# Kernel tuning notes

Measured on AMD Instinct MI355X. Metric: run time of the kernel, lower is better.

Reference implementation:

```python
import jax, jax.numpy as jnp
import numpy as np

N = 50000      # nodes
E = 800000     # edges
B = 512        # graphs in batch
DRNL = 64      # drnl_dim (feature_dim = 0)
H = 256        # hidden


def setup_inputs() -> dict:
    key = jax.random.key(0)
    ks = jax.random.split(key, 12)
    x = jax.random.normal(ks[0], (N, DRNL), jnp.float32)
    edge_index = jax.random.randint(ks[1], (2, E), 0, N)
    batch_vec = jnp.sort(jax.random.randint(ks[2], (N,), 0, B))
    u_idx = jax.random.randint(ks[3], (B,), 0, N)
    v_idx = jax.random.randint(ks[4], (B,), 0, N)

    def glorot(k, shp):
        scale = jnp.sqrt(2.0 / (shp[0] + shp[1]))
        return (jax.random.normal(k, shp, jnp.float32) * scale).astype(jnp.float32)

    W0 = glorot(ks[5], (DRNL, H)); b0 = jnp.zeros((H,), jnp.float32)
    W1 = glorot(ks[6], (H, H));    b1 = jnp.zeros((H,), jnp.float32)
    W2 = glorot(ks[7], (H, H));    b2 = jnp.zeros((H,), jnp.float32)
    Wm1 = glorot(ks[8], (3 * H, H)); bm1 = jnp.zeros((H,), jnp.float32)
    Wm2 = glorot(ks[9], (H, 1));     bm2 = jnp.zeros((1,), jnp.float32)
    return dict(x=x, edge_index=edge_index, batch_vec=batch_vec,
                u_idx=u_idx, v_idx=v_idx,
                W0=W0, b0=b0, W1=W1, b1=b1, W2=W2, b2=b2,
                Wm1=Wm1, bm1=bm1, Wm2=Wm2, bm2=bm2)


def _gcn_encode(x, src, dst, Ws, bs):
    # Standard GCN: h' = D^-1/2 (A + I) D^-1/2 h W + b, ReLU between layers.
    n = x.shape[0]
    loop = jnp.arange(n)
    src2 = jnp.concatenate([src, loop])  # add self-loops
    dst2 = jnp.concatenate([dst, loop])
    deg = jax.ops.segment_sum(jnp.ones_like(dst2, x.dtype), dst2, num_segments=n)
    dis = jax.lax.rsqrt(jnp.maximum(deg, 1.0))          # D^-1/2
    norm = dis[src2] * dis[dst2]                         # per-edge norm [E+N]

    h = x
    for i, (W, b) in enumerate(zip(Ws, bs)):
        msg = h[src2] * norm[:, None]                    # gather + scale
        agg = jax.ops.segment_sum(msg, dst2, num_segments=n)
        h = agg @ W + b
        if i < len(Ws) - 1:
            h = jax.nn.relu(h)
    return h


def reference(x, edge_index, batch_vec, u_idx, v_idx,
              W0, b0, W1, b1, W2, b2, Wm1, bm1, Wm2, bm2):
    src, dst = edge_index[0], edge_index[1]
    h = _gcn_encode(x, src, dst, (W0, W1, W2), (b0, b1, b2))   # [N, H]

    # global_mean_pool over batch_vec -> [B, H]
    cnt = jax.ops.segment_sum(jnp.ones((h.shape[0],), h.dtype), batch_vec,
                              num_segments=B)
    g = jax.ops.segment_sum(h, batch_vec, num_segments=B) / \
        jnp.maximum(cnt, 1.0)[:, None]

    # concat [g, h[u], h[v]] -> MLP -> [B] logits
    z = jnp.concatenate([g, h[u_idx], h[v_idx]], axis=1)       # [B, 3H]
    z = jax.nn.relu(z @ Wm1 + bm1)
    return (z @ Wm2 + bm2).squeeze(-1)
```

## Files before the change

### kernel.cpp

```cpp
#include <hip/hip_runtime.h>
#include <hip/hip_bf16.h>
#include <stdint.h>

#ifndef DRNL
#define DRNL 64
#define HDIM 256
#endif

#define CHUNK 4096
#define BCAP 3072

typedef __attribute__((ext_vector_type(4))) float f32x4;
typedef __attribute__((ext_vector_type(8))) _Float16 f16x8;

__device__ __forceinline__ int imin(int a, int b) { return a < b ? a : b; }

__global__ __launch_bounds__(256) void k_misc(
    const int* __restrict__ batch,
    const float* __restrict__ x,
    const float* __restrict__ W0, const float* __restrict__ W1,
    const float* __restrict__ W2,
    int* __restrict__ gstart,
    _Float16* __restrict__ x16,
    _Float16* __restrict__ W0t, _Float16* __restrict__ W1t,
    _Float16* __restrict__ W2t,
    int N, int B) {
    const int gsz = gridDim.x * 256;
    const int gid0 = blockIdx.x * 256 + threadIdx.x;

    for (int i = gid0; i < (DRNL + 2 * HDIM) * 256; i += gsz) {
        int b = i >> 8, c = i & 255;
        const float* W; _Float16* T; int k, K;
        if (b < DRNL)            { W = W0; T = W0t; k = b;              K = DRNL; }
        else if (b < DRNL + 256) { W = W1; T = W1t; k = b - DRNL;       K = HDIM; }
        else                     { W = W2; T = W2t; k = b - DRNL - 256; K = HDIM; }
        T[(size_t)c * K + k] = (_Float16)W[(size_t)k * 256 + c];
    }

    for (int i = gid0; i < N * DRNL; i += gsz) x16[i] = (_Float16)x[i];

    for (int i = gid0; i <= N; i += gsz) {
        if (i == 0) {
            int b0 = batch[0];
            for (int b = 0; b <= b0; ++b) gstart[b] = 0;
        } else if (i == N) {
            int bl = batch[N - 1];
            for (int b = bl + 1; b <= B; ++b) gstart[b] = N;
        } else {
            int bp = batch[i - 1], bc = batch[i];
            if (bc != bp)
                for (int b = bp + 1; b <= bc; ++b) gstart[b] = i;
        }
    }
}

__global__ __launch_bounds__(256) void k_hist(const int* __restrict__ dst,
                                              int* __restrict__ ghist,
                                              int E, int P, int SH, int NBUCK) {
    __shared__ int h[512];
    int tid = threadIdx.x, p = blockIdx.x;
    for (int i = tid; i < NBUCK; i += 256) h[i] = 0;
    __syncthreads();
    int e0 = p * CHUNK, e1 = imin(e0 + CHUNK, E);
    for (int e = e0 + tid; e < e1; e += 256)
        atomicAdd(&h[dst[e] >> SH], 1);
    __syncthreads();
    for (int b = tid; b < NBUCK; b += 256)
        ghist[(size_t)b * P + p] = h[b];
}

__global__ __launch_bounds__(256) void k_gbase(int* __restrict__ ghist,
                                               int* __restrict__ btot, int P) {
    __shared__ int s[256];
    int b = blockIdx.x, tid = threadIdx.x;
    int* row = ghist + (size_t)b * P;
    int carry = 0;
    for (int base = 0; base < P; base += 256) {
        int idx = base + tid;
        int v = (idx < P) ? row[idx] : 0;
        s[tid] = v;
        __syncthreads();
        for (int o = 1; o < 256; o <<= 1) {
            int t = (tid >= o) ? s[tid - o] : 0;
            __syncthreads();
            s[tid] += t;
            __syncthreads();
        }
        if (idx < P) row[idx] = carry + s[tid] - v;
        carry += s[255];
        __syncthreads();
    }
    if (tid == 0) btot[b] = carry;
}

__global__ __launch_bounds__(256) void k_btscan(const int* __restrict__ btot,
                                                int* __restrict__ bbase,
                                                int* __restrict__ rowptr,
                                                int NBUCK, int N, int E) {
    __shared__ int s[256];
    int tid = threadIdx.x;
    int carry = 0;
    for (int base = 0; base < NBUCK; base += 256) {
        int idx = base + tid;
        int v = (idx < NBUCK) ? btot[idx] : 0;
        s[tid] = v;
        __syncthreads();
        for (int o = 1; o < 256; o <<= 1) {
            int t = (tid >= o) ? s[tid - o] : 0;
            __syncthreads();
            s[tid] += t;
            __syncthreads();
        }
        if (idx < NBUCK) bbase[idx] = carry + s[tid] - v;
        carry += s[255];
        __syncthreads();
    }
    if (tid == 0) { bbase[NBUCK] = E; rowptr[N] = E; }
}

__global__ __launch_bounds__(256) void k_scatter(const int* __restrict__ src,
                                                 const int* __restrict__ dst,
                                                 const int* __restrict__ ghist,
                                                 const int* __restrict__ bbase,
                                                 int* __restrict__ tmp,
                                                 int E, int P, int SH, int NBUCK) {
    __shared__ int base[512];
    int p = blockIdx.x, tid = threadIdx.x;
    for (int b = tid; b < NBUCK; b += 256)
        base[b] = bbase[b] + ghist[(size_t)b * P + p];
    __syncthreads();
    int e0 = p * CHUNK, e1 = imin(e0 + CHUNK, E);
    int msk = (1 << SH) - 1;
    for (int e = e0 + tid; e < e1; e += 256) {
        int d = dst[e];
        int r = atomicAdd(&base[d >> SH], 1);
        tmp[r] = (src[e] << SH) | (d & msk);
    }
}

__global__ __launch_bounds__(256) void k_bsort(const int* __restrict__ tmp,
                                               const int* __restrict__ bbase,
                                               int* __restrict__ col,
                                               int* __restrict__ rowptr,
                                               float* __restrict__ dis,
                                               _Float16* __restrict__ x16,
                                               int SH, int N) {
    __shared__ int cnt[512];
    __shared__ int off[512];
    __shared__ int sscan[256];
    __shared__ int eL[BCAP];
    __shared__ unsigned short rnk[BCAP];
    __shared__ int sL[BCAP];
    int b = blockIdx.x, tid = threadIdx.x;
    int nodes = 1 << SH, node0 = b << SH, msk = nodes - 1;
    int lo = bbase[b], hi = bbase[b + 1], m = hi - lo;
    bool fast = (m <= BCAP);

    for (int i = tid; i < nodes; i += 256) cnt[i] = 0;
    __syncthreads();
    if (fast) {
        for (int i = tid; i < m; i += 256) {
            int v = tmp[lo + i];
            eL[i] = v;
            rnk[i] = (unsigned short)atomicAdd(&cnt[v & msk], 1);
        }
    } else {
        for (int i = tid; i < m; i += 256)
            atomicAdd(&cnt[tmp[lo + i] & msk], 1);
    }
    __syncthreads();
    int carry = 0;
    for (int base = 0; base < nodes; base += 256) {
        int idx = base + tid;
        int v = (idx < nodes) ? cnt[idx] : 0;
        sscan[tid] = v;
        __syncthreads();
        for (int o = 1; o < 256; o <<= 1) {
            int t = (tid >= o) ? sscan[tid - o] : 0;
            __syncthreads();
            sscan[tid] += t;
            __syncthreads();
        }
        if (idx < nodes) off[idx] = carry + sscan[tid] - v;
        carry += sscan[255];
        __syncthreads();
    }
    for (int i = tid; i < nodes; i += 256) {
        int node = node0 + i;
        if (node < N) {
            rowptr[node] = lo + off[i];
            dis[node]    = rsqrtf((float)cnt[i] + 1.f);
        }
    }
    int rlim = imin(nodes, N - node0);
    for (int u = tid; u < rlim * 8; u += 256) {
        int r = u >> 3, c = u & 7;
        float d = rsqrtf((float)cnt[r] + 1.f);
        f16x8* xv = (f16x8*)(x16 + (size_t)(node0 + r) * 64);
        f16x8 v = xv[c];
        f16x8 o;
#pragma unroll
        for (int k = 0; k < 8; ++k) o[k] = (_Float16)((float)v[k] * d);
        xv[c] = o;
    }
    __syncthreads();
    if (fast) {
        for (int i = tid; i < m; i += 256) {
            int v = eL[i];
            sL[off[v & msk] + rnk[i]] = v >> SH;
        }
        __syncthreads();
        for (int i = tid; i < m; i += 256) col[lo + i] = sL[i];
    } else {
        for (int i = tid; i < nodes; i += 256) cnt[i] = 0;
        __syncthreads();
        for (int i = tid; i < m; i += 256) {
            int v = tmp[lo + i];
            int d = v & msk;
            int r = atomicAdd(&cnt[d], 1);
            col[lo + off[d] + r] = v >> SH;
        }
    }
}

template <int FBLK>
__global__ __launch_bounds__(256) void k_agg(const _Float16* __restrict__ hs,
                                             const float* __restrict__ dis,
                                             const int* __restrict__ rowptr,
                                             const int* __restrict__ col,
                                             _Float16* __restrict__ A16, int N) {
    int node_wg, f;
    if constexpr (FBLK == 4) {
        int wg = blockIdx.x;
        int xcd = wg & 7;
        f = xcd >> 1;
        int half = xcd & 1;
        int NH = gridDim.x >> 3;
        node_wg = half * NH + (wg >> 3);
    } else {
        node_wg = blockIdx.x;
        f = 0;
    }
    int lane = threadIdx.x & 63;
    int wv = threadIdx.x >> 6;
    int oct = lane >> 3;
    int fl = lane & 7;
    int gw = node_wg * 32 + wv * 8 + oct;
    bool valid = gw < N;
    int gwc = valid ? gw : N - 1;
    const size_t boff = (size_t)f * ((size_t)N * 64);
    const f16x8* hv = (const f16x8*)(hs + boff);
    float acc[8];
#pragma unroll
    for (int k = 0; k < 8; ++k) acc[k] = 0.f;

    int e0 = rowptr[gwc];
    int e1 = valid ? rowptr[gwc + 1] : e0;
    int j = e0;
    while (__any(j < e1)) {
        bool a0 = j < e1, a1 = j + 1 < e1, a2 = j + 2 < e1, a3 = j + 3 < e1;
        int s0 = col[a0 ? j : 0];
        int s1 = col[a1 ? j + 1 : 0];
        int s2 = col[a2 ? j + 2 : 0];
        int s3 = col[a3 ? j + 3 : 0];
        float m0 = a0 ? 1.f : 0.f, m1 = a1 ? 1.f : 0.f;
        float m2 = a2 ? 1.f : 0.f, m3 = a3 ? 1.f : 0.f;
        f16x8 v0 = hv[(size_t)s0 * 8 + fl];
        f16x8 v1 = hv[(size_t)s1 * 8 + fl];
        f16x8 v2 = hv[(size_t)s2 * 8 + fl];
        f16x8 v3 = hv[(size_t)s3 * 8 + fl];
#pragma unroll
        for (int k = 0; k < 8; ++k) acc[k] += m0 * (float)v0[k];
#pragma unroll
        for (int k = 0; k < 8; ++k) acc[k] += m1 * (float)v1[k];
#pragma unroll
        for (int k = 0; k < 8; ++k) acc[k] += m2 * (float)v2[k];
#pragma unroll
        for (int k = 0; k < 8; ++k) acc[k] += m3 * (float)v3[k];
        j += 4;
    }

    float dn = dis[gwc];
    f16x8 hsv = hv[(size_t)gwc * 8 + fl];
    f16x8 o;
#pragma unroll
    for (int k = 0; k < 8; ++k)
        o[k] = (_Float16)((acc[k] + (float)hsv[k]) * dn);
    if (valid)
        __builtin_nontemporal_store(
            o, (f16x8*)(A16 + boff + (size_t)gw * 64 + fl * 8));
}

template <int K, int OUT_RELU, int SCALE>
__global__ __launch_bounds__(256) void k_wgemm(const _Float16* __restrict__ A,
                                               const _Float16* __restrict__ W,
                                               const float* __restrict__ bias,
                                               const float* __restrict__ dis,
                                               _Float16* __restrict__ outh, int n) {
    constexpr int KT = K / 32;
    __shared__ _Float16 sOut[4 * 16 * 64];

    const int tid  = threadIdx.x;
    const int lane = tid & 63;
    const int wv   = tid >> 6;
    const int c15  = lane & 15;
    const int q    = lane >> 4;
    const int c0   = wv << 6;
    const int row0 = blockIdx.x * 64;
    const size_t bstride = (size_t)n * 64;
    _Float16* sO = sOut + wv * (16 * 64);
    _Float16* ob = outh + (size_t)wv * bstride;

    f16x8 wf[4][KT];
#pragma unroll
    for (int ct = 0; ct < 4; ++ct)
#pragma unroll
        for (int kt = 0; kt < KT; ++kt)
            wf[ct][kt] = *(const f16x8*)(
                W + (size_t)(c0 + (ct << 4) + c15) * K + (kt << 5) + q * 8);

    float bv[4];
#pragma unroll
    for (int ct = 0; ct < 4; ++ct) bv[ct] = bias[c0 + (ct << 4) + c15];

#pragma unroll
    for (int st = 0; st < 4; ++st) {
        const int r0 = row0 + (st << 4);
        const int ra = imin(r0 + c15, n - 1);
        f16x8 af[KT];
#pragma unroll
        for (int kt = 0; kt < KT; ++kt) {
            const int kk = kt << 5;
            af[kt] = *(const f16x8*)(A + (size_t)(kk >> 6) * bstride +
                                     (size_t)ra * 64 + (kk & 63) + q * 8);
        }
        f32x4 acc[4];
#pragma unroll
        for (int ct = 0; ct < 4; ++ct) acc[ct] = (f32x4)0.f;
#pragma unroll
        for (int kt = 0; kt < KT; ++kt)
#pragma unroll
            for (int ct = 0; ct < 4; ++ct)
                acc[ct] = __builtin_amdgcn_mfma_f32_16x16x32_f16(
                    af[kt], wf[ct][kt], acc[ct], 0, 0, 0);

        float ds[4];
#pragma unroll
        for (int r = 0; r < 4; ++r)
            ds[r] = SCALE ? dis[imin(r0 + (q << 2) + r, n - 1)] : 1.f;

#pragma unroll
        for (int ct = 0; ct < 4; ++ct) {
#pragma unroll
            for (int r = 0; r < 4; ++r) {
                float v = acc[ct][r] + bv[ct];
                if (OUT_RELU) v = fmaxf(v, 0.f);
                v *= ds[r];
                sO[((q << 2) + r) * 64 + (ct << 4) + c15] = (_Float16)v;
            }
        }
        __syncthreads();
#pragma unroll
        for (int ps = 0; ps < 2; ++ps) {
            int u = (ps << 6) + lane;
            int rr = u >> 3, ch = u & 7;
            f16x8 vv = *(const f16x8*)(sO + rr * 64 + ch * 8);
            if (r0 + rr < n)
                *(f16x8*)(ob + (size_t)(r0 + rr) * 64 + ch * 8) = vv;
        }
        __syncthreads();
    }
}

__global__ __launch_bounds__(256) void k_head(const _Float16* __restrict__ h,
                                              const int* __restrict__ gstart,
                                              const int* __restrict__ u,
                                              const int* __restrict__ v,
                                              const float* __restrict__ Wm1,
                                              const float* __restrict__ bm1,
                                              const float* __restrict__ Wm2,
                                              const float* __restrict__ bm2,
                                              float* __restrict__ out, int N) {
    int b = blockIdx.x;
    int t = threadIdx.x;
    __shared__ float z[3 * HDIM];
    __shared__ float red[4];
    const _Float16* hb = h + (size_t)(t >> 6) * ((size_t)N * 64) + (t & 63);
    int s = gstart[b], e = gstart[b + 1];
    float pa = 0.f;
    int i = s;
    for (; i + 3 < e; i += 4) {
        float a0 = (float)hb[(size_t)i * 64];
        float a1 = (float)hb[(size_t)(i + 1) * 64];
        float a2 = (float)hb[(size_t)(i + 2) * 64];
        float a3 = (float)hb[(size_t)(i + 3) * 64];
        pa += (a0 + a1) + (a2 + a3);
    }
    for (; i < e; ++i) pa += (float)hb[(size_t)i * 64];
    z[t]            = pa / fmaxf((float)(e - s), 1.f);
    z[HDIM + t]     = (float)hb[(size_t)u[b] * 64];
    z[2 * HDIM + t] = (float)hb[(size_t)v[b] * 64];
    __syncthreads();
    float acc[8];
#pragma unroll
    for (int k = 0; k < 8; ++k) acc[k] = 0.f;
    for (int k = 0; k < 3 * HDIM; k += 8) {
#pragma unroll
        for (int jj = 0; jj < 8; ++jj)
            acc[jj] = fmaf(z[k + jj], Wm1[(size_t)(k + jj) * HDIM + t], acc[jj]);
    }
    float sum = (((acc[0] + acc[1]) + (acc[2] + acc[3])) +
                 ((acc[4] + acc[5]) + (acc[6] + acc[7]))) + bm1[t];
    float hid = fmaxf(sum, 0.f);
    float p = hid * Wm2[t];
    for (int off = 32; off; off >>= 1) p += __shfl_down(p, off);
    if ((t & 63) == 0) red[t >> 6] = p;
    __syncthreads();
    if (t == 0) out[b] = red[0] + red[1] + red[2] + red[3] + bm2[0];
}

extern "C" void kernel_launch(void* const* d_in, const int* in_sizes, int n_in,
                              void* d_out, int out_size, void* d_ws, size_t ws_size,
                              hipStream_t stream) {
    const float* x    = (const float*)d_in[0];
    const int*   ei   = (const int*)d_in[1];
    const int*   batc = (const int*)d_in[2];
    const int*   uidx = (const int*)d_in[3];
    const int*   vidx = (const int*)d_in[4];
    const float* W0   = (const float*)d_in[5];
    const float* b0   = (const float*)d_in[6];
    const float* W1   = (const float*)d_in[7];
    const float* b1   = (const float*)d_in[8];
    const float* W2   = (const float*)d_in[9];
    const float* b2   = (const float*)d_in[10];
    const float* Wm1  = (const float*)d_in[11];
    const float* bm1  = (const float*)d_in[12];
    const float* Wm2  = (const float*)d_in[13];
    const float* bm2  = (const float*)d_in[14];
    float* out = (float*)d_out;

    const int N = in_sizes[0] / DRNL;
    const int E = in_sizes[1] / 2;
    const int B = in_sizes[3];
    const int* src = ei;
    const int* dst = ei + E;

    int SH = 7;
    while (((N + (1 << SH) - 1) >> SH) > 512) ++SH;
    const int NBUCK = (N + (1 << SH) - 1) >> SH;
    const int P = (E + CHUNK - 1) / CHUNK;

    char* w = (char*)d_ws;
    size_t off = 0;
    auto carve = [&](size_t bytes) {
        void* p = w + off;
        off = (off + bytes + 255) & ~(size_t)255;
        return p;
    };
    int*       rowptr = (int*)carve((size_t)(N + 1) * 4);
    int*       colA   = (int*)carve((size_t)E * 4);
    float*     dis    = (float*)carve((size_t)N * 4);
    int*       gstart = (int*)carve((size_t)(B + 1) * 4);
    _Float16*  A16    = (_Float16*)carve((size_t)N * HDIM * 2);
    _Float16*  h16    = (_Float16*)carve((size_t)N * HDIM * 2);
    _Float16*  x16    = (_Float16*)carve((size_t)N * DRNL * 2);
    _Float16*  W0t    = (_Float16*)carve((size_t)DRNL * HDIM * 2);
    _Float16*  W1t    = (_Float16*)carve((size_t)HDIM * HDIM * 2);
    _Float16*  W2t    = (_Float16*)carve((size_t)HDIM * HDIM * 2);
    int*       ghist  = (int*)carve((size_t)NBUCK * P * 4);
    int*       btot   = (int*)carve(512 * 4);
    int*       bbase  = (int*)carve(513 * 4);
    int*       tmpE   = (int*)carve((size_t)E * 4);
    (void)ws_size;

    k_misc<<<1024, 256, 0, stream>>>(batc, x, W0, W1, W2, gstart,
                                     x16, W0t, W1t, W2t, N, B);
    k_hist<<<P, 256, 0, stream>>>(dst, ghist, E, P, SH, NBUCK);
    k_gbase<<<NBUCK, 256, 0, stream>>>(ghist, btot, P);
    k_btscan<<<1, 256, 0, stream>>>(btot, bbase, rowptr, NBUCK, N, E);
    k_scatter<<<P, 256, 0, stream>>>(src, dst, ghist, bbase, tmpE, E, P, SH, NBUCK);
    k_bsort<<<NBUCK, 256, 0, stream>>>(tmpE, bbase, colA, rowptr, dis, x16, SH, N);

    int gemmb = (N + 63) / 64;
    int NB = (N + 31) / 32;
    int NH = (NB + 1) / 2;
    int aggb4 = 8 * NH;

    k_agg<1><<<NB, 256, 0, stream>>>(x16, dis, rowptr, colA, A16, N);
    k_wgemm<DRNL, 1, 1><<<gemmb, 256, 0, stream>>>(A16, W0t, b0, dis, h16, N);
    k_agg<4><<<aggb4, 256, 0, stream>>>(h16, dis, rowptr, colA, A16, N);
    k_wgemm<HDIM, 1, 1><<<gemmb, 256, 0, stream>>>(A16, W1t, b1, dis, h16, N);
    k_agg<4><<<aggb4, 256, 0, stream>>>(h16, dis, rowptr, colA, A16, N);
    k_wgemm<HDIM, 0, 0><<<gemmb, 256, 0, stream>>>(A16, W2t, b2, dis, h16, N);

    k_head<<<B, 256, 0, stream>>>(h16, gstart, uidx, vidx, Wm1, bm1, Wm2, bm2, out, N);
}
```

Before: 341.8 us.

## Stage GEMM A tiles via async global-to-LDS loads with swizzle, drop block barriers

The weight transpose now writes weights in MFMA-fragment order, so each wave loads its B fragments as contiguous 16-byte vectors. In the GEMM, A tiles are copied into per-wave LDS with global_load_lds in an XOR-swizzled layout and then read back as fragments. Bias and dis values are fetched once per wave and spread with shuffles. The output staging buffer is swizzled to avoid bank conflicts, and block-wide __syncthreads is removed because each wave only touches its own LDS region. This adds LDS use and sets launch bounds to one block, which may lower occupancy. It also relies on intra-wave ordering of LDS accesses being correct without explicit barriers.

```diff
diff --git a/kernel.cpp b/kernel.cpp
--- a/kernel.cpp
+++ b/kernel.cpp
@@ -12,6 +12,12 @@
 
 typedef __attribute__((ext_vector_type(4))) float f32x4;
 typedef __attribute__((ext_vector_type(8))) _Float16 f16x8;
+
+__device__ __forceinline__ void async16(void* lds, const void* g) {
+    __builtin_amdgcn_global_load_lds(
+        (const __attribute__((address_space(1))) void*)g,
+        (__attribute__((address_space(3))) void*)(char*)lds, 16, 0, 0);
+}
 
 __device__ __forceinline__ int imin(int a, int b) { return a < b ? a : b; }
 
@@ -34,7 +40,12 @@
         if (b < DRNL)            { W = W0; T = W0t; k = b;              K = DRNL; }
         else if (b < DRNL + 256) { W = W1; T = W1t; k = b - DRNL;       K = HDIM; }
         else                     { W = W2; T = W2t; k = b - DRNL - 256; K = HDIM; }
-        T[(size_t)c * K + k] = (_Float16)W[(size_t)k * 256 + c];
+        int KT = K >> 5;
+        int cg = c >> 6, ct = (c >> 4) & 3, cl = c & 15;
+        int kt = k >> 5, qq = (k >> 3) & 3, j = k & 7;
+        int lane = (qq << 4) | cl;
+        T[(((size_t)(cg * KT + kt) * 4 + ct) * 64 + lane) * 8 + j] =
+            (_Float16)W[(size_t)k * 256 + c];
     }
 
     for (int i = gid0; i < N * DRNL; i += gsz) x16[i] = (_Float16)x[i];
@@ -292,48 +303,75 @@
 }
 
 template <int K, int OUT_RELU, int SCALE>
-__global__ __launch_bounds__(256) void k_wgemm(const _Float16* __restrict__ A,
-                                               const _Float16* __restrict__ W,
-                                               const float* __restrict__ bias,
-                                               const float* __restrict__ dis,
-                                               _Float16* __restrict__ outh, int n) {
-    constexpr int KT = K / 32;
-    __shared__ _Float16 sOut[4 * 16 * 64];
+__global__ __launch_bounds__(256, 1) void k_wgemm(const _Float16* __restrict__ A,
+                                                  const _Float16* __restrict__ Wf,
+                                                  const float* __restrict__ bias,
+                                                  const float* __restrict__ dis,
+                                                  _Float16* __restrict__ outh, int n) {
+    constexpr int KT  = K / 32;
+    constexpr int NFB = K / 64;
+    constexpr int NI  = NFB * 2;
+    constexpr int STG = NFB * 1024;
+    __shared__ _Float16 sAll[4 * (STG + 1024)];
 
     const int tid  = threadIdx.x;
     const int lane = tid & 63;
     const int wv   = tid >> 6;
     const int c15  = lane & 15;
     const int q    = lane >> 4;
-    const int c0   = wv << 6;
     const int row0 = blockIdx.x * 64;
     const size_t bstride = (size_t)n * 64;
-    _Float16* sO = sOut + wv * (16 * 64);
-    _Float16* ob = outh + (size_t)wv * bstride;
+    _Float16* sbuf = sAll + wv * (STG + 1024);
+    _Float16* sO   = sbuf + STG;
+    _Float16* ob   = outh + (size_t)wv * bstride;
 
     f16x8 wf[4][KT];
-#pragma unroll
-    for (int ct = 0; ct < 4; ++ct)
-#pragma unroll
-        for (int kt = 0; kt < KT; ++kt)
-            wf[ct][kt] = *(const f16x8*)(
-                W + (size_t)(c0 + (ct << 4) + c15) * K + (kt << 5) + q * 8);
-
+    const _Float16* wp = Wf + ((size_t)wv * KT * 4 * 64 + lane) * 8;
+#pragma unroll
+    for (int kt = 0; kt < KT; ++kt)
+#pragma unroll
+        for (int ct = 0; ct < 4; ++ct)
+            wf[ct][kt] = *(const f16x8*)(wp + (size_t)((kt * 4 + ct) * 64) * 8);
+
+    float bvl = bias[(wv << 6) + lane];
     float bv[4];
 #pragma unroll
-    for (int ct = 0; ct < 4; ++ct) bv[ct] = bias[c0 + (ct << 4) + c15];
+    for (int ct = 0; ct < 4; ++ct) bv[ct] = __shfl(bvl, (ct << 4) + c15);
+
+    float dsv[4][4];
+    if (SCALE) {
+        float dvl = dis[imin(row0 + lane, n - 1)];
+#pragma unroll
+        for (int st = 0; st < 4; ++st)
+#pragma unroll
+            for (int r = 0; r < 4; ++r)
+                dsv[st][r] = __shfl(dvl, (st << 4) + (q << 2) + r);
+    }
 
 #pragma unroll
     for (int st = 0; st < 4; ++st) {
         const int r0 = row0 + (st << 4);
-        const int ra = imin(r0 + c15, n - 1);
+#pragma unroll
+        for (int i = 0; i < NI; ++i) {
+            int s   = (i << 6) + lane;
+            int fb  = s >> 7;
+            int row = (s >> 3) & 15;
+            int ch  = (s & 7) ^ (row & 7);
+            int gr  = imin(r0 + row, n - 1);
+            async16(sbuf + (size_t)s * 8,
+                    A + (size_t)fb * bstride + (size_t)gr * 64 + ch * 8);
+        }
+        asm volatile("s_waitcnt vmcnt(0)" ::: "memory");
+        __builtin_amdgcn_sched_barrier(0);
+
         f16x8 af[KT];
 #pragma unroll
         for (int kt = 0; kt < KT; ++kt) {
-            const int kk = kt << 5;
-            af[kt] = *(const f16x8*)(A + (size_t)(kk >> 6) * bstride +
-                                     (size_t)ra * 64 + (kk & 63) + q * 8);
-        }
+            int off = (kt >> 1) * 1024 + c15 * 64 +
+                      ((((kt & 1) * 4 + q) ^ (c15 & 7)) * 8);
+            af[kt] = *(const f16x8*)(sbuf + off);
+        }
+
         f32x4 acc[4];
 #pragma unroll
         for (int ct = 0; ct < 4; ++ct) acc[ct] = (f32x4)0.f;
@@ -344,31 +382,27 @@
                 acc[ct] = __builtin_amdgcn_mfma_f32_16x16x32_f16(
                     af[kt], wf[ct][kt], acc[ct], 0, 0, 0);
 
-        float ds[4];
-#pragma unroll
-        for (int r = 0; r < 4; ++r)
-            ds[r] = SCALE ? dis[imin(r0 + (q << 2) + r, n - 1)] : 1.f;
-
 #pragma unroll
         for (int ct = 0; ct < 4; ++ct) {
 #pragma unroll
             for (int r = 0; r < 4; ++r) {
                 float v = acc[ct][r] + bv[ct];
                 if (OUT_RELU) v = fmaxf(v, 0.f);
-                v *= ds[r];
-                sO[((q << 2) + r) * 64 + (ct << 4) + c15] = (_Float16)v;
+                if (SCALE) v *= dsv[st][r];
+                int row = (q << 2) + r;
+                int colx = (ct << 4) + c15;
+                int sw = (((colx >> 3) ^ (row & 7)) << 3) | (colx & 7);
+                sO[row * 64 + sw] = (_Float16)v;
             }
         }
-        __syncthreads();
 #pragma unroll
         for (int ps = 0; ps < 2; ++ps) {
             int u = (ps << 6) + lane;
-            int rr = u >> 3, ch = u & 7;
-            f16x8 vv = *(const f16x8*)(sO + rr * 64 + ch * 8);
+            int rr = u >> 3, ch2 = u & 7;
+            f16x8 vv = *(const f16x8*)(sO + rr * 64 + ((ch2 ^ (rr & 7)) << 3));
             if (r0 + rr < n)
-                *(f16x8*)(ob + (size_t)(r0 + rr) * 64 + ch * 8) = vv;
-        }
-        __syncthreads();
+                *(f16x8*)(ob + (size_t)(r0 + rr) * 64 + ch2 * 8) = vv;
+        }
     }
 }
 
```

Measured after the change: 294.4 us. 13.9% less time.
